# Performance work log

Hardware: AMD Instinct MI355X
Metric: run time of the kernel (lower is better)

## Reference

```python
import jax, jax.numpy as jnp
import numpy as np

DIM, NH, NKV = 1024, 16, 4
HD = DIM // NH  # 64
B, T = 2, 2048


def _rotary_freqs(seq_len, dim):
    inv_freq = 1.0 / (10000.0 ** (jnp.arange(0, dim, 2, dtype=jnp.float32) / dim))
    pos = jnp.arange(seq_len, dtype=jnp.float32)
    return pos[:, None] * inv_freq[None, :]  # [T, dim/2]


def _apply_rotary(x, freqs):
    # x: [B, H, T, HD]; freqs: [T, HD/2]
    x1, x2 = x[..., ::2], x[..., 1::2]
    cos, sin = jnp.cos(freqs), jnp.sin(freqs)
    # NOTE: faithful to source, second half is x1*sin - x2*cos (not +)
    return jnp.concatenate([x1 * cos - x2 * sin, x1 * sin - x2 * cos], axis=-1)


def setup_inputs() -> dict:
    key = jax.random.key(0)
    ks = jax.random.split(key, 5)
    s = 0.02
    return {
        "x": jax.random.normal(ks[0], (B, T, DIM), dtype=jnp.float32),
        "Wq": jax.random.normal(ks[1], (DIM, DIM), dtype=jnp.float32) * s,
        "bq": jnp.zeros((DIM,), jnp.float32),
        "Wk": jax.random.normal(ks[2], (DIM, NKV * HD), dtype=jnp.float32) * s,
        "bk": jnp.zeros((NKV * HD,), jnp.float32),
        "Wv": jax.random.normal(ks[3], (DIM, NKV * HD), dtype=jnp.float32) * s,
        "bv": jnp.zeros((NKV * HD,), jnp.float32),
        "Wo": jax.random.normal(ks[4], (DIM, DIM), dtype=jnp.float32) * s,
        "bo": jnp.zeros((DIM,), jnp.float32),
    }


def reference(x, Wq, bq, Wk, bk, Wv, bv, Wo, bo):
    Bx, Tx, C = x.shape
    q = (x @ Wq + bq).reshape(Bx, Tx, NH, HD).transpose(0, 2, 1, 3)   # [B,NH,T,HD]
    k = (x @ Wk + bk).reshape(Bx, Tx, NKV, HD).transpose(0, 2, 1, 3)  # [B,NKV,T,HD]
    v = (x @ Wv + bv).reshape(Bx, Tx, NKV, HD).transpose(0, 2, 1, 3)

    freqs = _rotary_freqs(Tx, HD)
    q = _apply_rotary(q, freqs)
    k = _apply_rotary(k, freqs)

    rep = NH // NKV
    k = jnp.repeat(k, rep, axis=1)  # [B,NH,T,HD]
    v = jnpp = jnp.repeat(v, rep, axis=1)

    scores = jnp.einsum('bhqd,bhkd->bhqk', q, k) / jnp.sqrt(jnp.float32(HD))
    causal = jnp.tril(jnp.ones((Tx, Tx), dtype=bool))
    scores = jnp.where(causal[None, None], scores, -jnp.inf)
    attn = jax.nn.softmax(scores, axis=-1)
    ctx = jnp.einsum('bhqk,bhkd->bhqd', attn, v)
    out = ctx.transpose(0, 2, 1, 3).reshape(Bx, Tx, C)
    return out @ Wo + bo
```

## Files before the change

kernel.cpp:

```cpp
#include <hip/hip_runtime.h>
#include <math.h>

#define DIM 1024
#define NH 16
#define NKV 4
#define HD 64
#define HALF 32
#define NB 2
#define SEQ 2048
#define KVD 256
#define MTOT 4096
#define QSCALE 0.18033688f
#define MBIAS 8.0f

typedef __bf16 bf16x8 __attribute__((ext_vector_type(8)));
typedef float f32x4 __attribute__((ext_vector_type(4)));
typedef unsigned short u16x8 __attribute__((ext_vector_type(8)));

#define MFMA16(a, b, c) __builtin_amdgcn_mfma_f32_16x16x32_bf16(a, b, c, 0, 0, 0)

__device__ __forceinline__ unsigned short f2bf(float f) {
    unsigned int u = __float_as_uint(f);
    u = (u + 0x7fffu + ((u >> 16) & 1u)) >> 16;
    return (unsigned short)u;
}

__device__ __forceinline__ unsigned cvt_pk(float lo, float hi) {
    unsigned r;
    asm("v_cvt_pk_bf16_f32 %0, %1, %2" : "=v"(r) : "v"(lo), "v"(hi));
    return r;
}

__device__ __forceinline__ void gll16(const unsigned short* g, unsigned short* l) {
    __builtin_amdgcn_global_load_lds((const __attribute__((address_space(1))) void*)g,
                                     (__attribute__((address_space(3))) void*)l, 16, 0, 0);
}

__global__ __launch_bounds__(256) void prep_kernel(
    const float* __restrict__ x,
    const float* __restrict__ Wq, const float* __restrict__ Wk,
    const float* __restrict__ Wv, const float* __restrict__ Wo,
    unsigned short* __restrict__ xb,
    unsigned short* __restrict__ qt, unsigned short* __restrict__ kt,
    unsigned short* __restrict__ vt, unsigned short* __restrict__ ot,
    float* __restrict__ cosb, float* __restrict__ sinb)
{
    __shared__ float tile[64][65];
    const int bx = blockIdx.x;
    const int tid = threadIdx.x;
    if (bx < 256) {
        int idx = bx * 256 + tid;
        int t = idx >> 5, d = idx & 31;
        float e = (float)(2 * d) / (float)HD;
        float invf = 1.0f / powf(10000.0f, e);
        float f = (float)t * invf;
        cosb[idx] = cosf(f);
        sinb[idx] = sinf(f);
    } else if (bx < 2304) {
        int i = ((bx - 256) * 256 + tid) * 8;
        float4 v0 = *(const float4*)&x[i];
        float4 v1 = *(const float4*)&x[i + 4];
        u16x8 o;
        o[0] = f2bf(v0.x); o[1] = f2bf(v0.y); o[2] = f2bf(v0.z); o[3] = f2bf(v0.w);
        o[4] = f2bf(v1.x); o[5] = f2bf(v1.y); o[6] = f2bf(v1.z); o[7] = f2bf(v1.w);
        *(u16x8*)&xb[i] = o;
    } else {
        int idx2 = bx - 2304;
        int z = idx2 >> 8, rem = idx2 & 255, xx = rem & 15, yy = rem >> 4;
        const float* W; unsigned short* Wt; int N;
        switch (z) {
            case 0: W = Wq; Wt = qt; N = DIM; break;
            case 1: W = Wk; Wt = kt; N = KVD; break;
            case 2: W = Wv; Wt = vt; N = KVD; break;
            default: W = Wo; Wt = ot; N = DIM; break;
        }
        const int n0 = xx * 64;
        if (n0 >= N) return;
        const int k0 = yy * 64;
        const int row = tid >> 2, coff = (tid & 3) * 16;
#pragma unroll
        for (int i = 0; i < 4; i++) {
            float4 v = *(const float4*)&W[(size_t)(k0 + row) * N + n0 + coff + i * 4];
            tile[row][coff + i * 4 + 0] = v.x; tile[row][coff + i * 4 + 1] = v.y;
            tile[row][coff + i * 4 + 2] = v.z; tile[row][coff + i * 4 + 3] = v.w;
        }
        __syncthreads();
        u16x8 a, b;
#pragma unroll
        for (int i = 0; i < 8; i++) a[i] = f2bf(tile[coff + i][row]);
#pragma unroll
        for (int i = 0; i < 8; i++) b[i] = f2bf(tile[coff + 8 + i][row]);
        *(u16x8*)&Wt[(size_t)(n0 + row) * DIM + k0 + coff] = a;
        *(u16x8*)&Wt[(size_t)(n0 + row) * DIM + k0 + coff + 8] = b;
    }
}

__global__ __launch_bounds__(256) void qkv_gemm_kernel(
    const unsigned short* __restrict__ xb,
    const unsigned short* __restrict__ wqt, const unsigned short* __restrict__ wkt,
    const unsigned short* __restrict__ wvt,
    const float* __restrict__ bq, const float* __restrict__ bk, const float* __restrict__ bv,
    const float* __restrict__ cosb, const float* __restrict__ sinb,
    unsigned short* __restrict__ qbuf, unsigned short* __restrict__ kbuf,
    unsigned short* __restrict__ vT)
{
    __shared__ unsigned short As[64 * 64];
    __shared__ unsigned short Bs[128 * 64];
    const int tid = threadIdx.x;
    const int lane = tid & 63, w = tid >> 6;
    const int l15 = lane & 15, lg = lane >> 4;
    const int bid = blockIdx.x;
    const int lid = (bid & 7) * 96 + (bid >> 3);
    const int m0 = (lid / 12) * 64;
    const int n0g = (lid % 12) * 128;

    const unsigned short* Wt; const float* bias; int n0, mode;
    if (n0g < DIM)            { Wt = wqt; bias = bq; n0 = n0g; mode = 0; }
    else if (n0g < DIM + KVD) { Wt = wkt; bias = bk; n0 = n0g - DIM; mode = 1; }
    else                      { Wt = wvt; bias = bv; n0 = n0g - DIM - KVD; mode = 2; }

    const int wr = w >> 1, wc = w & 1;

    f32x4 acc[2][4];
#pragma unroll
    for (int i = 0; i < 2; i++)
#pragma unroll
        for (int j = 0; j < 4; j++) acc[i][j] = (f32x4){0.f, 0.f, 0.f, 0.f};

    for (int k0 = 0; k0 < DIM; k0 += 64) {
        __syncthreads();
#pragma unroll
        for (int i = 0; i < 2; i++) {
            int S = i * 256 + tid;
            int r = S >> 3, qd = S & 7;
            gll16(xb + (size_t)(m0 + r) * DIM + k0 + ((qd ^ (r & 7)) * 8),
                  &As[(i * 256 + (tid & ~63)) * 8]);
        }
#pragma unroll
        for (int i = 0; i < 4; i++) {
            int S = i * 256 + tid;
            int r = S >> 3, qd = S & 7;
            gll16(Wt + (size_t)(n0 + r) * DIM + k0 + ((qd ^ (r & 7)) * 8),
                  &Bs[(i * 256 + (tid & ~63)) * 8]);
        }
        __syncthreads();
        bf16x8 af[2][2], bfr[4][2];
#pragma unroll
        for (int r = 0; r < 2; r++) {
            const int row = wr * 32 + r * 16 + l15;
#pragma unroll
            for (int kk = 0; kk < 2; kk++)
                af[r][kk] = *(const bf16x8*)&As[row * 64 + (((kk * 4 + lg) ^ (row & 7)) << 3)];
        }
#pragma unroll
        for (int c = 0; c < 4; c++) {
            const int row = wc * 64 + c * 16 + l15;
#pragma unroll
            for (int kk = 0; kk < 2; kk++)
                bfr[c][kk] = *(const bf16x8*)&Bs[row * 64 + (((kk * 4 + lg) ^ (row & 7)) << 3)];
        }
#pragma unroll
        for (int kk = 0; kk < 2; kk++)
#pragma unroll
            for (int r = 0; r < 2; r++)
#pragma unroll
                for (int c = 0; c < 4; c++)
                    acc[r][c] = MFMA16(af[r][kk], bfr[c][kk], acc[r][c]);
    }

    const int nloc = n0 + wc * 64;
    const bool even = (l15 & 1) == 0;
#pragma unroll
    for (int rt = 0; rt < 2; rt++) {
#pragma unroll
        for (int ct = 0; ct < 4; ct++) {
            const int c = ct * 16 + l15;
            const float bsv = bias[nloc + c];
            if (mode == 2) {
                const int col = nloc + c;
                const int khh = col >> 6, d = col & 63;
                const int bb = m0 >> 11;
                const int t = (m0 & (SEQ - 1)) + wr * 32 + rt * 16 + lg * 4;
                float v0 = acc[rt][ct][0] + bsv;
                float v1 = acc[rt][ct][1] + bsv;
                float v2 = acc[rt][ct][2] + bsv;
                float v3 = acc[rt][ct][3] + bsv;
                unsigned short* dst = vT + ((size_t)(bb * NKV + khh) * 64 + d) * SEQ + t;
                *(uint2*)dst = make_uint2(cvt_pk(v0, v1), cvt_pk(v2, v3));
            } else {
                const int p = c >> 1;
#pragma unroll
                for (int q = 0; q < 4; q++) {
                    const int mrow = m0 + wr * 32 + rt * 16 + lg * 4 + q;
                    float val = acc[rt][ct][q] + bsv;
                    float prt = __shfl_xor(val, 1);
                    const int t = mrow & (SEQ - 1);
                    float cs = cosb[t * HALF + p];
                    float sn = sinb[t * HALF + p];
                    float outv = even ? (val * cs - prt * sn) : (prt * sn - val * cs);
                    int outc = even ? p : (p + 32);
                    if (mode == 0) qbuf[(size_t)mrow * DIM + nloc + outc] = f2bf(outv * QSCALE);
                    else           kbuf[(size_t)mrow * KVD + nloc + outc] = f2bf(outv);
                }
            }
        }
    }
}

__global__ __launch_bounds__(512) void attn_mfma_kernel(
    const unsigned short* __restrict__ qb, const unsigned short* __restrict__ kb,
    const unsigned short* __restrict__ vT, unsigned short* __restrict__ ctx)
{
    __shared__ unsigned short Ks[2][64 * 64];
    __shared__ unsigned short Vt[2][64 * 64];
    __shared__ unsigned Pw[8][16 * 32];

    const int tid = threadIdx.x;
    const int lane = tid & 63, w = tid >> 6;
    const int l15 = lane & 15, lg = lane >> 4;
    const int h = blockIdx.y;
    const int b = blockIdx.z;
    const int kh = h >> 2;
    const int g = h + NH * b;
    const int v = (blockIdx.x + g + 8 * (g >> 4)) & 15;
    const int T = (v >> 3) ? (15 - (v & 7)) : v;
    const int q0 = T * 128;

    const unsigned short* kg = kb + (size_t)b * SEQ * KVD + (size_t)kh * HD;
    const unsigned short* vg = vT + ((size_t)(b * NKV + kh) * HD) * SEQ;

    const int qg_row = q0 + 16 * w + l15;
    const int swzd = (l15 & 7) << 3;
    unsigned* PW = &Pw[w][l15 * 32];
    const int pswz = (l15 & 7) << 2;

    const unsigned short* qptr = qb + (size_t)(b * SEQ + qg_row) * DIM + h * HD + lg * 8;
    bf16x8 bq0 = *(const bf16x8*)qptr;
    bf16x8 bq1 = *(const bf16x8*)(qptr + 32);

    const int r1 = tid >> 3, d81 = ((tid & 7) ^ (r1 & 7)) * 8;

    gll16(kg + (size_t)r1 * KVD + d81, &Ks[0][(w * 64) * 8]);
    gll16(vg + (size_t)r1 * SEQ + d81, &Vt[0][(w * 64) * 8]);
    __syncthreads();

    f32x4 o[4];
#pragma unroll
    for (int i = 0; i < 4; i++) o[i] = (f32x4){0.f, 0.f, 0.f, 0.f};
    float lrun = 0.f;

    const int nch = 2 * T + 2;
    const int wmax = q0 + 16 * w + 15;
    const int wmin = q0 + 16 * w;
#pragma unroll 1
    for (int ch = 0; ch < nch; ch++) {
        const int cur = ch & 1;
        if (ch + 1 < nch) {
            const int kv1 = (ch + 1) * 64;
            gll16(kg + (size_t)(kv1 + r1) * KVD + d81, &Ks[cur ^ 1][(w * 64) * 8]);
            gll16(vg + (size_t)r1 * SEQ + kv1 + d81,   &Vt[cur ^ 1][(w * 64) * 8]);
        }

        if (64 * ch <= wmax) {
            f32x4 sacc[4];
#pragma unroll
            for (int i = 0; i < 4; i++) sacc[i] = (f32x4){0.f, 0.f, 0.f, 0.f};
            __builtin_amdgcn_s_setprio(1);
#pragma unroll
            for (int ct = 0; ct < 4; ct++) {
                const int kr = ct * 16 + l15;
                bf16x8 ak = *(const bf16x8*)&Ks[cur][kr * 64 + ((lg * 8) ^ swzd)];
                sacc[ct] = MFMA16(ak, bq0, sacc[ct]);
            }
#pragma unroll
            for (int ct = 0; ct < 4; ct++) {
                const int kr = ct * 16 + l15;
                bf16x8 ak = *(const bf16x8*)&Ks[cur][kr * 64 + ((32 + lg * 8) ^ swzd)];
                sacc[ct] = MFMA16(ak, bq1, sacc[ct]);
            }
            __builtin_amdgcn_s_setprio(0);

            if (64 * ch + 63 > wmin) {
#pragma unroll
                for (int ct = 0; ct < 4; ct++)
#pragma unroll
                    for (int r = 0; r < 4; r++)
                        if (64 * ch + ct * 16 + lg * 4 + r > qg_row) sacc[ct][r] = -INFINITY;
            }

            float rs = 0.f;
            unsigned pk0[4], pk1[4];
#pragma unroll
            for (int ct = 0; ct < 4; ct++) {
                float p0 = exp2f(sacc[ct][0] - MBIAS);
                float p1 = exp2f(sacc[ct][1] - MBIAS);
                float p2 = exp2f(sacc[ct][2] - MBIAS);
                float p3 = exp2f(sacc[ct][3] - MBIAS);
                rs += (p0 + p1) + (p2 + p3);
                pk0[ct] = cvt_pk(p0, p1);
                pk1[ct] = cvt_pk(p2, p3);
            }
            lrun += rs;

#pragma unroll
            for (int ct = 0; ct < 4; ct++) {
                int wrd = (ct * 8 + lg * 2) ^ pswz;
                *(uint2*)&PW[wrd] = make_uint2(pk0[ct], pk1[ct]);
            }

            __builtin_amdgcn_s_setprio(1);
#pragma unroll
            for (int s = 0; s < 2; s++) {
                int wrd = (s * 16 + lg * 4) ^ pswz;
                bf16x8 ap = *(const bf16x8*)&PW[wrd];
#pragma unroll
                for (int dt = 0; dt < 4; dt++) {
                    const int d = dt * 16 + l15;
                    bf16x8 bv2 = *(const bf16x8*)&Vt[cur][d * 64 + ((s * 32 + lg * 8) ^ ((d & 7) << 3))];
                    o[dt] = MFMA16(ap, bv2, o[dt]);
                }
            }
            __builtin_amdgcn_s_setprio(0);
        }

        __syncthreads();
    }

    lrun += __shfl_xor(lrun, 16);
    lrun += __shfl_xor(lrun, 32);
    float linv = 1.0f / lrun;
    float lb0 = __shfl(linv, lg * 4 + 0);
    float lb1 = __shfl(linv, lg * 4 + 1);
    float lb2 = __shfl(linv, lg * 4 + 2);
    float lb3 = __shfl(linv, lg * 4 + 3);
#pragma unroll
    for (int dt = 0; dt < 4; dt++) {
        const size_t base = (size_t)(b * SEQ + q0 + 16 * w + lg * 4) * DIM + h * HD + dt * 16 + l15;
        ctx[base]           = f2bf(o[dt][0] * lb0);
        ctx[base + DIM]     = f2bf(o[dt][1] * lb1);
        ctx[base + 2 * DIM] = f2bf(o[dt][2] * lb2);
        ctx[base + 3 * DIM] = f2bf(o[dt][3] * lb3);
    }
}

__global__ __launch_bounds__(256) void outproj_kernel(
    const unsigned short* __restrict__ ctx, const unsigned short* __restrict__ wot,
    const float* __restrict__ bo, float* __restrict__ out)
{
    __shared__ unsigned short As[64 * 64];
    __shared__ unsigned short Bs[128 * 64];
    const int tid = threadIdx.x;
    const int lane = tid & 63, w = tid >> 6;
    const int l15 = lane & 15, lg = lane >> 4;
    const int bid = blockIdx.x;
    const int lid = (bid & 7) * 64 + (bid >> 3);
    const int m0 = (lid >> 3) * 64;
    const int n0 = (lid & 7) * 128;
    const int wr = w >> 1, wc = w & 1;

    f32x4 acc[2][4];
#pragma unroll
    for (int i = 0; i < 2; i++)
#pragma unroll
        for (int j = 0; j < 4; j++) acc[i][j] = (f32x4){0.f, 0.f, 0.f, 0.f};

    for (int k0 = 0; k0 < DIM; k0 += 64) {
        __syncthreads();
#pragma unroll
        for (int i = 0; i < 2; i++) {
            int S = i * 256 + tid;
            int r = S >> 3, qd = S & 7;
            gll16(ctx + (size_t)(m0 + r) * DIM + k0 + ((qd ^ (r & 7)) * 8),
                  &As[(i * 256 + (tid & ~63)) * 8]);
        }
#pragma unroll
        for (int i = 0; i < 4; i++) {
            int S = i * 256 + tid;
            int r = S >> 3, qd = S & 7;
            gll16(wot + (size_t)(n0 + r) * DIM + k0 + ((qd ^ (r & 7)) * 8),
                  &Bs[(i * 256 + (tid & ~63)) * 8]);
        }
        __syncthreads();
        bf16x8 af[2][2], bfr[4][2];
#pragma unroll
        for (int r = 0; r < 2; r++) {
            const int row = wr * 32 + r * 16 + l15;
#pragma unroll
            for (int kk = 0; kk < 2; kk++)
                af[r][kk] = *(const bf16x8*)&As[row * 64 + (((kk * 4 + lg) ^ (row & 7)) << 3)];
        }
#pragma unroll
        for (int c = 0; c < 4; c++) {
            const int row = wc * 64 + c * 16 + l15;
#pragma unroll
            for (int kk = 0; kk < 2; kk++)
                bfr[c][kk] = *(const bf16x8*)&Bs[row * 64 + (((kk * 4 + lg) ^ (row & 7)) << 3)];
        }
#pragma unroll
        for (int kk = 0; kk < 2; kk++)
#pragma unroll
            for (int r = 0; r < 2; r++)
#pragma unroll
                for (int c = 0; c < 4; c++)
                    acc[r][c] = MFMA16(af[r][kk], bfr[c][kk], acc[r][c]);
    }

#pragma unroll
    for (int rt = 0; rt < 2; rt++) {
#pragma unroll
        for (int ct = 0; ct < 4; ct++) {
            const int ncol = n0 + wc * 64 + ct * 16 + l15;
            const float bsv = bo[ncol];
#pragma unroll
            for (int q = 0; q < 4; q++) {
                const int mrow = m0 + wr * 32 + rt * 16 + lg * 4 + q;
                out[(size_t)mrow * DIM + ncol] = acc[rt][ct][q] + bsv;
            }
        }
    }
}

extern "C" void kernel_launch(void* const* d_in, const int* in_sizes, int n_in,
                              void* d_out, int out_size, void* d_ws, size_t ws_size,
                              hipStream_t stream) {
    (void)in_sizes; (void)n_in; (void)out_size; (void)ws_size;
    const float* x  = (const float*)d_in[0];
    const float* Wq = (const float*)d_in[1];
    const float* bq = (const float*)d_in[2];
    const float* Wk = (const float*)d_in[3];
    const float* bk = (const float*)d_in[4];
    const float* Wv = (const float*)d_in[5];
    const float* bv = (const float*)d_in[6];
    const float* Wo = (const float*)d_in[7];
    const float* bo = (const float*)d_in[8];
    float* out = (float*)d_out;
    char* ws = (char*)d_ws;

    unsigned short* xb  = (unsigned short*)(ws);
    unsigned short* qbf = (unsigned short*)(ws + 8388608);
    unsigned short* kbf = (unsigned short*)(ws + 16777216);
    unsigned short* ctx = (unsigned short*)(ws + 20971520);
    unsigned short* wqt = (unsigned short*)(ws + 29360128);
    unsigned short* wkt = (unsigned short*)(ws + 31457280);
    unsigned short* wvt = (unsigned short*)(ws + 31981568);
    unsigned short* wot = (unsigned short*)(ws + 32505856);
    float* cosb = (float*)(ws + 34603008);
    float* sinb = (float*)(ws + 34865152);
    unsigned short* vTb = (unsigned short*)(ws + 35127296);

    hipLaunchKernelGGL(prep_kernel, dim3(3328), dim3(256), 0, stream,
                       x, Wq, Wk, Wv, Wo, xb, wqt, wkt, wvt, wot, cosb, sinb);
    hipLaunchKernelGGL(qkv_gemm_kernel, dim3(768), dim3(256), 0, stream,
                       xb, wqt, wkt, wvt, bq, bk, bv, cosb, sinb, qbf, kbf, vTb);
    hipLaunchKernelGGL(attn_mfma_kernel, dim3(16, NH, NB), dim3(512), 0, stream,
                       qbf, kbf, vTb, ctx);
    hipLaunchKernelGGL(outproj_kernel, dim3(512), dim3(256), 0, stream,
                       ctx, wot, bo, out);
}
```

Baseline: 95.49 us.

## Switch attention to 32x32x16 MFMA with register-resident P via permlane32 swap

Rewrites the attention kernel to use 32x32x16 bf16 MFMAs with 4 waves of 32 query rows each, instead of 8 waves of 16 rows using 16x16x32 MFMAs. The P matrix is rearranged in registers with v_permlane32_swap, which removes the per-wave LDS scratch buffer and its write/read round trip. Each thread now issues two async K/V loads per tile, and causal masking is limited to the last two chunks. This trades more accumulator registers and fewer waves per block for fewer LDS accesses and larger MFMA tiles.

Result: slower. 99.93 us (+4.6%).

```diff
diff --git a/kernel.cpp b/kernel.cpp
--- a/kernel.cpp
+++ b/kernel.cpp
@@ -15,9 +15,12 @@
 
 typedef __bf16 bf16x8 __attribute__((ext_vector_type(8)));
 typedef float f32x4 __attribute__((ext_vector_type(4)));
+typedef float f32x16 __attribute__((ext_vector_type(16)));
+typedef unsigned u32x4 __attribute__((ext_vector_type(4)));
 typedef unsigned short u16x8 __attribute__((ext_vector_type(8)));
 
 #define MFMA16(a, b, c) __builtin_amdgcn_mfma_f32_16x16x32_bf16(a, b, c, 0, 0, 0)
+#define MFMA32(a, b, c) __builtin_amdgcn_mfma_f32_32x32x16_bf16(a, b, c, 0, 0, 0)
 
 __device__ __forceinline__ unsigned short f2bf(float f) {
     unsigned int u = __float_as_uint(f);
@@ -29,6 +32,10 @@
     unsigned r;
     asm("v_cvt_pk_bf16_f32 %0, %1, %2" : "=v"(r) : "v"(lo), "v"(hi));
     return r;
+}
+
+__device__ __forceinline__ void pl32swap(unsigned &dst, unsigned &src) {
+    asm volatile("v_permlane32_swap_b32 %0, %1" : "+v"(dst), "+v"(src));
 }
 
 __device__ __forceinline__ void gll16(const unsigned short* g, unsigned short* l) {
@@ -207,51 +214,51 @@
     }
 }
 
-__global__ __launch_bounds__(512) void attn_mfma_kernel(
+__global__ __launch_bounds__(256, 2) void attn_mfma_kernel(
     const unsigned short* __restrict__ qb, const unsigned short* __restrict__ kb,
     const unsigned short* __restrict__ vT, unsigned short* __restrict__ ctx)
 {
     __shared__ unsigned short Ks[2][64 * 64];
     __shared__ unsigned short Vt[2][64 * 64];
-    __shared__ unsigned Pw[8][16 * 32];
 
     const int tid = threadIdx.x;
     const int lane = tid & 63, w = tid >> 6;
-    const int l15 = lane & 15, lg = lane >> 4;
+    const int l31 = lane & 31, b5 = lane >> 5;
     const int h = blockIdx.y;
     const int b = blockIdx.z;
     const int kh = h >> 2;
     const int g = h + NH * b;
     const int v = (blockIdx.x + g + 8 * (g >> 4)) & 15;
-    const int T = (v >> 3) ? (15 - (v & 7)) : v;
+    const int T = (v >> 3) ? (15 - (v & 7)) : (v & 7);
     const int q0 = T * 128;
 
     const unsigned short* kg = kb + (size_t)b * SEQ * KVD + (size_t)kh * HD;
     const unsigned short* vg = vT + ((size_t)(b * NKV + kh) * HD) * SEQ;
 
-    const int qg_row = q0 + 16 * w + l15;
-    const int swzd = (l15 & 7) << 3;
-    unsigned* PW = &Pw[w][l15 * 32];
-    const int pswz = (l15 & 7) << 2;
-
-    const unsigned short* qptr = qb + (size_t)(b * SEQ + qg_row) * DIM + h * HD + lg * 8;
-    bf16x8 bq0 = *(const bf16x8*)qptr;
-    bf16x8 bq1 = *(const bf16x8*)(qptr + 32);
-
-    const int r1 = tid >> 3, d81 = ((tid & 7) ^ (r1 & 7)) * 8;
+    const int qrow = q0 + 32 * w + l31;
+    const unsigned short* qptr = qb + (size_t)(b * SEQ + qrow) * DIM + h * HD + 8 * b5;
+    bf16x8 bq[4];
+#pragma unroll
+    for (int kk = 0; kk < 4; kk++) bq[kk] = *(const bf16x8*)(qptr + 16 * kk);
+
+    const int S1 = tid, r1 = S1 >> 3, d81 = ((S1 & 7) ^ (r1 & 7)) * 8;
+    const int S2 = 256 + tid, r2 = S2 >> 3, d82 = ((S2 & 7) ^ (r2 & 7)) * 8;
 
     gll16(kg + (size_t)r1 * KVD + d81, &Ks[0][(w * 64) * 8]);
     gll16(vg + (size_t)r1 * SEQ + d81, &Vt[0][(w * 64) * 8]);
+    gll16(kg + (size_t)r2 * KVD + d82, &Ks[0][(256 + w * 64) * 8]);
+    gll16(vg + (size_t)r2 * SEQ + d82, &Vt[0][(256 + w * 64) * 8]);
     __syncthreads();
 
-    f32x4 o[4];
-#pragma unroll
-    for (int i = 0; i < 4; i++) o[i] = (f32x4){0.f, 0.f, 0.f, 0.f};
+    f32x16 o[2];
+#pragma unroll
+    for (int dt = 0; dt < 2; dt++)
+#pragma unroll
+        for (int i = 0; i < 16; i++) o[dt][i] = 0.f;
     float lrun = 0.f;
 
     const int nch = 2 * T + 2;
-    const int wmax = q0 + 16 * w + 15;
-    const int wmin = q0 + 16 * w;
+    const int wmax = q0 + 32 * w + 31;
 #pragma unroll 1
     for (int ch = 0; ch < nch; ch++) {
         const int cur = ch & 1;
@@ -259,87 +266,86 @@
             const int kv1 = (ch + 1) * 64;
             gll16(kg + (size_t)(kv1 + r1) * KVD + d81, &Ks[cur ^ 1][(w * 64) * 8]);
             gll16(vg + (size_t)r1 * SEQ + kv1 + d81,   &Vt[cur ^ 1][(w * 64) * 8]);
+            gll16(kg + (size_t)(kv1 + r2) * KVD + d82, &Ks[cur ^ 1][(256 + w * 64) * 8]);
+            gll16(vg + (size_t)r2 * SEQ + kv1 + d82,   &Vt[cur ^ 1][(256 + w * 64) * 8]);
         }
 
         if (64 * ch <= wmax) {
-            f32x4 sacc[4];
-#pragma unroll
-            for (int i = 0; i < 4; i++) sacc[i] = (f32x4){0.f, 0.f, 0.f, 0.f};
+            f32x16 sacc[2];
+#pragma unroll
+            for (int kt = 0; kt < 2; kt++)
+#pragma unroll
+                for (int i = 0; i < 16; i++) sacc[kt][i] = 0.f;
             __builtin_amdgcn_s_setprio(1);
 #pragma unroll
-            for (int ct = 0; ct < 4; ct++) {
-                const int kr = ct * 16 + l15;
-                bf16x8 ak = *(const bf16x8*)&Ks[cur][kr * 64 + ((lg * 8) ^ swzd)];
-                sacc[ct] = MFMA16(ak, bq0, sacc[ct]);
-            }
-#pragma unroll
-            for (int ct = 0; ct < 4; ct++) {
-                const int kr = ct * 16 + l15;
-                bf16x8 ak = *(const bf16x8*)&Ks[cur][kr * 64 + ((32 + lg * 8) ^ swzd)];
-                sacc[ct] = MFMA16(ak, bq1, sacc[ct]);
-            }
-            __builtin_amdgcn_s_setprio(0);
-
-            if (64 * ch + 63 > wmin) {
-#pragma unroll
-                for (int ct = 0; ct < 4; ct++)
-#pragma unroll
-                    for (int r = 0; r < 4; r++)
-                        if (64 * ch + ct * 16 + lg * 4 + r > qg_row) sacc[ct][r] = -INFINITY;
-            }
-
-            float rs = 0.f;
-            unsigned pk0[4], pk1[4];
-#pragma unroll
-            for (int ct = 0; ct < 4; ct++) {
-                float p0 = exp2f(sacc[ct][0] - MBIAS);
-                float p1 = exp2f(sacc[ct][1] - MBIAS);
-                float p2 = exp2f(sacc[ct][2] - MBIAS);
-                float p3 = exp2f(sacc[ct][3] - MBIAS);
-                rs += (p0 + p1) + (p2 + p3);
-                pk0[ct] = cvt_pk(p0, p1);
-                pk1[ct] = cvt_pk(p2, p3);
-            }
-            lrun += rs;
-
-#pragma unroll
-            for (int ct = 0; ct < 4; ct++) {
-                int wrd = (ct * 8 + lg * 2) ^ pswz;
-                *(uint2*)&PW[wrd] = make_uint2(pk0[ct], pk1[ct]);
-            }
-
-            __builtin_amdgcn_s_setprio(1);
-#pragma unroll
-            for (int s = 0; s < 2; s++) {
-                int wrd = (s * 16 + lg * 4) ^ pswz;
-                bf16x8 ap = *(const bf16x8*)&PW[wrd];
-#pragma unroll
-                for (int dt = 0; dt < 4; dt++) {
-                    const int d = dt * 16 + l15;
-                    bf16x8 bv2 = *(const bf16x8*)&Vt[cur][d * 64 + ((s * 32 + lg * 8) ^ ((d & 7) << 3))];
-                    o[dt] = MFMA16(ap, bv2, o[dt]);
+            for (int kt = 0; kt < 2; kt++) {
+                const int row = kt * 32 + l31;
+#pragma unroll
+                for (int kk = 0; kk < 4; kk++) {
+                    bf16x8 ak = *(const bf16x8*)&Ks[cur][row * 64 + (((2 * kk + b5) ^ (row & 7)) << 3)];
+                    sacc[kt] = MFMA32(ak, bq[kk], sacc[kt]);
                 }
             }
             __builtin_amdgcn_s_setprio(0);
-        }
-
-        __syncthreads();
-    }
-
-    lrun += __shfl_xor(lrun, 16);
+
+            if (ch >= nch - 2) {
+#pragma unroll
+                for (int kt = 0; kt < 2; kt++)
+#pragma unroll
+                    for (int reg = 0; reg < 16; reg++) {
+                        int keyg = 64 * ch + 32 * kt + (reg & 3) + 8 * (reg >> 2) + 4 * b5;
+                        if (keyg > qrow) sacc[kt][reg] = -INFINITY;
+                    }
+            }
+
+            float rs = 0.f;
+            unsigned pkw[2][8];
+#pragma unroll
+            for (int kt = 0; kt < 2; kt++)
+#pragma unroll
+                for (int idx = 0; idx < 8; idx++) {
+                    int rg = (idx >> 1) * 4 + (idx & 1) * 2;
+                    float pa = exp2f(sacc[kt][rg] - MBIAS);
+                    float pb = exp2f(sacc[kt][rg + 1] - MBIAS);
+                    rs += pa + pb;
+                    pkw[kt][idx] = cvt_pk(pa, pb);
+                }
+            lrun += rs;
+
+            __builtin_amdgcn_s_setprio(1);
+#pragma unroll
+            for (int kk = 0; kk < 4; kk++) {
+                const int kt = kk >> 1, kl = kk & 1;
+                unsigned X0 = pkw[kt][(2 * kl + 1) * 2 + 0];
+                unsigned Y0 = pkw[kt][(2 * kl) * 2 + 0];
+                unsigned X1 = pkw[kt][(2 * kl + 1) * 2 + 1];
+                unsigned Y1 = pkw[kt][(2 * kl) * 2 + 1];
+                pl32swap(Y0, X0);
+                pl32swap(Y1, X1);
+                u32x4 av = {Y0, Y1, X0, X1};
+                bf16x8 ap = __builtin_bit_cast(bf16x8, av);
+#pragma unroll
+                for (int dt = 0; dt < 2; dt++) {
+                    const int row = dt * 32 + l31;
+                    bf16x8 bv2 = *(const bf16x8*)&Vt[cur][row * 64 + (((2 * kk + b5) ^ (row & 7)) << 3)];
+                    o[dt] = MFMA32(ap, bv2, o[dt]);
+                }
+            }
+            __builtin_amdgcn_s_setprio(0);
+        }
+
+        __syncthreads();
+    }
+
     lrun += __shfl_xor(lrun, 32);
     float linv = 1.0f / lrun;
-    float lb0 = __shfl(linv, lg * 4 + 0);
-    float lb1 = __shfl(linv, lg * 4 + 1);
-    float lb2 = __shfl(linv, lg * 4 + 2);
-    float lb3 = __shfl(linv, lg * 4 + 3);
-#pragma unroll
-    for (int dt = 0; dt < 4; dt++) {
-        const size_t base = (size_t)(b * SEQ + q0 + 16 * w + lg * 4) * DIM + h * HD + dt * 16 + l15;
-        ctx[base]           = f2bf(o[dt][0] * lb0);
-        ctx[base + DIM]     = f2bf(o[dt][1] * lb1);
-        ctx[base + 2 * DIM] = f2bf(o[dt][2] * lb2);
-        ctx[base + 3 * DIM] = f2bf(o[dt][3] * lb3);
+#pragma unroll
+    for (int reg = 0; reg < 16; reg++) {
+        const int ql = (reg & 3) + 8 * (reg >> 2) + 4 * b5;
+        float lb = __shfl(linv, ql);
+        const size_t rowoff = (size_t)(b * SEQ + q0 + 32 * w + ql) * DIM + h * HD + l31;
+        ctx[rowoff]      = f2bf(o[0][reg] * lb);
+        ctx[rowoff + 32] = f2bf(o[1][reg] * lb);
     }
 }
 
@@ -452,7 +458,7 @@
                        x, Wq, Wk, Wv, Wo, xb, wqt, wkt, wvt, wot, cosb, sinb);
     hipLaunchKernelGGL(qkv_gemm_kernel, dim3(768), dim3(256), 0, stream,
                        xb, wqt, wkt, wvt, bq, bk, bv, cosb, sinb, qbf, kbf, vTb);
-    hipLaunchKernelGGL(attn_mfma_kernel, dim3(16, NH, NB), dim3(512), 0, stream,
+    hipLaunchKernelGGL(attn_mfma_kernel, dim3(16, NH, NB), dim3(256), 0, stream,
                        qbf, kbf, vTb, ctx);
     hipLaunchKernelGGL(outproj_kernel, dim3(512), dim3(256), 0, stream,
                        ctx, wot, bo, out);
```
